# Kernel tuning notes

Measured on AMD Instinct MI355X. Metric: run time of the kernel, lower is better.

The kernel has to match this reference:

```python
import jax, jax.numpy as jnp
import numpy as np

STRIDE = 2
PADDING = (1, 1)
OUT_PADDING = (0, 0)


def conv_transpose2d(x, weight, bias, stride, padding, out_padding):
    # weight: (Cin, Cout, kh, kw) -- torch ConvTranspose2d layout.
    # The original code does: stride-insert zeros, zero-pad by (k-1), append
    # out_padding rows/cols, valid-conv with the spatially-flipped kernel,
    # then crop `padding` from each side. That is exactly a dilated conv:
    kh, kw = weight.shape[2], weight.shape[3]
    w = jnp.flip(weight, (2, 3)).transpose(1, 0, 2, 3)  # (Cout, Cin, kh, kw)
    pad = ((kh - 1 - padding[0], kh - 1 - padding[0] + out_padding[0]),
           (kw - 1 - padding[1], kw - 1 - padding[1] + out_padding[1]))
    out = jax.lax.conv_general_dilated(
        x, w,
        window_strides=(1, 1),
        padding=pad,
        lhs_dilation=(stride, stride),
        dimension_numbers=('NCHW', 'OIHW', 'NCHW'))
    return out + bias[None, :, None, None]


def setup_inputs() -> dict:
    key = jax.random.key(0)
    k1, k2, k3 = jax.random.split(key, 3)
    Cin, Cout, kh, kw = 256, 128, 4, 4
    bnd = (1.0 / (Cin * kh * kw)) ** 0.5  # matches uniform_(-k**0.5, k**0.5)
    x = jax.random.normal(k1, (16, Cin, 64, 64), dtype=jnp.float32)
    weight = jax.random.uniform(k2, (Cin, Cout, kh, kw), jnp.float32, -bnd, bnd)
    bias = jax.random.uniform(k3, (Cout,), jnp.float32, -bnd, bnd)
    return {"x": x, "weight": weight, "bias": bias}


def reference(x, weight, bias):
    # Output: (16, 128, 128, 128) = (H-1)*2 - 2*1 + 4
    return conv_transpose2d(x, weight, bias, STRIDE, PADDING, OUT_PADDING)
```

## Files before the change

### kernel.cpp

```cpp
#include <hip/hip_runtime.h>
#include <stdint.h>

typedef unsigned short u16;
typedef __bf16 bf16x8 __attribute__((ext_vector_type(8)));
typedef float f32x4 __attribute__((ext_vector_type(4)));
typedef float f32x2 __attribute__((ext_vector_type(2)));

static const size_t XT_BYTES = (size_t)16 * 66 * 66 * 256 * 2;
static const size_t WK_BYTES = (size_t)2 * 2 * 8 * 2 * 2 * 128 * 32 * 2;

__device__ __forceinline__ u16 f2bf(float f) {
  unsigned u = __float_as_uint(f);
  unsigned r = (u + 0x7fff + ((u >> 16) & 1)) >> 16;
  return (u16)r;
}

__device__ __forceinline__ void ld_g2l16(const u16* g, void* l) {
  __builtin_amdgcn_global_load_lds(
      (const __attribute__((address_space(1))) unsigned int*)(uintptr_t)g,
      (__attribute__((address_space(3))) unsigned int*)(unsigned int)(uintptr_t)l,
      16, 0, 0);
}

__device__ __forceinline__ int swz4(int row) { return (row ^ (row >> 2)) & 3; }

__global__ __launch_bounds__(256) void prep_all(const float* __restrict__ x,
                                                const float* __restrict__ w,
                                                u16* __restrict__ xt,
                                                u16* __restrict__ wk) {
  __shared__ __align__(16) u16 sh[64 * 264];
  const int t = threadIdx.x;
  const int bx = blockIdx.x;
  if (bx >= 1056) {
    int id = (bx - 1056) * 256 + t;
    int ci5 = id & 31;
    int co = (id >> 5) & 127;
    int q = (id >> 12) & 1;
    int dw = (id >> 13) & 1;
    int kc = (id >> 14) & 7;
    int dh = (id >> 17) & 1;
    int p = id >> 18;
    int ci = kc * 32 + ci5;
    int kh = 2 * dh + 1 - p;
    int kw = 2 * dw + 1 - q;
    wk[id] = f2bf(w[((ci * 128 + co) * 4 + kh) * 4 + kw]);
    return;
  }
  const int n = bx / 66;
  const int ihp = bx - n * 66;
  u16* xtn = xt + ((size_t)(n * 66 + ihp)) * 66 * 256;
  if (ihp == 0 || ihp == 65) {
    for (int j = 0; j < 9; ++j) {
      int idx = j * 256 + t;
      if (idx < 2112) ((uint4*)xtn)[idx] = make_uint4(0, 0, 0, 0);
    }
    return;
  }
  const int ih = ihp - 1;
  const int iw0 = (t & 15) * 4;
  const int cb = (t >> 4) * 4;
  const int swz = (t & 3) << 3;
  const float* xb = x + (size_t)n * 1048576 + (size_t)ih * 64 + iw0;
#pragma unroll
  for (int it = 0; it < 4; ++it) {
    int ci0 = it * 64 + cb;
    float4 v0 = *(const float4*)(xb + (size_t)(ci0 + 0) * 4096);
    float4 v1 = *(const float4*)(xb + (size_t)(ci0 + 1) * 4096);
    float4 v2 = *(const float4*)(xb + (size_t)(ci0 + 2) * 4096);
    float4 v3 = *(const float4*)(xb + (size_t)(ci0 + 3) * 4096);
    int col = ci0 ^ swz;
    ushort4 u;
    u.x = f2bf(v0.x); u.y = f2bf(v1.x); u.z = f2bf(v2.x); u.w = f2bf(v3.x);
    *(ushort4*)&sh[(iw0 + 0) * 264 + col] = u;
    u.x = f2bf(v0.y); u.y = f2bf(v1.y); u.z = f2bf(v2.y); u.w = f2bf(v3.y);
    *(ushort4*)&sh[(iw0 + 1) * 264 + col] = u;
    u.x = f2bf(v0.z); u.y = f2bf(v1.z); u.z = f2bf(v2.z); u.w = f2bf(v3.z);
    *(ushort4*)&sh[(iw0 + 2) * 264 + col] = u;
    u.x = f2bf(v0.w); u.y = f2bf(v1.w); u.z = f2bf(v2.w); u.w = f2bf(v3.w);
    *(ushort4*)&sh[(iw0 + 3) * 264 + col] = u;
  }
  __syncthreads();
#pragma unroll
  for (int j = 0; j < 8; ++j) {
    int idx = j * 256 + t;
    int iw = idx >> 5;
    int chunk = idx & 31;
    uint4 v = *(const uint4*)&sh[iw * 264 + ((chunk ^ ((iw >> 2) & 3)) << 3)];
    *(uint4*)&xtn[(size_t)(iw + 1) * 256 + chunk * 8] = v;
  }
  if (t < 64) {
    int iwp = (t >> 5) * 65;
    int chunk = t & 31;
    *(uint4*)&xtn[(size_t)iwp * 256 + chunk * 8] = make_uint4(0, 0, 0, 0);
  }
}

__global__ __launch_bounds__(512, 2) void gemm_ct(const u16* __restrict__ xt,
                                                  const u16* __restrict__ wk,
                                                  const float* __restrict__ bias,
                                                  float* __restrict__ out) {
  __shared__ __align__(16) u16 As[2][16384];
  __shared__ __align__(16) u16 Bs[2][8448];
  const int t = threadIdx.x;
  const int lane = t & 63;
  const int wv = t >> 6;
  const int wm = wv >> 2, wr = wv & 3;
  const int quad = lane >> 4, l15 = lane & 15;

  const int id = blockIdx.x;
  const int sid = (id & 7) * 64 + (id >> 3);
  const int mt = sid & 15;
  const int n = (sid >> 4) & 15;
  const int p = sid >> 8;
  const int m0 = mt * 4;

  const u16* wkp = wk + (size_t)p * 262144;
  const u16* xtn = xt + (size_t)n * (66 * 66 * 256);

  int aoffs[4];
#pragma unroll
  for (int it = 0; it < 4; ++it) {
    int c = it * 512 + t;
    int rr = c >> 2;
    aoffs[it] = rr * 32 + ((c & 3) ^ swz4(rr & 127)) * 8;
  }
  int bsrc[3];
#pragma unroll
  for (int it = 0; it < 3; ++it) {
    int c = it * 512 + t;
    int rr = c / 264;
    int rem = c - 264 * rr;
    int iwp = rem >> 2;
    bsrc[it] = rr * 16896 + iwp * 256 + ((rem & 3) ^ swz4(iwp)) * 8;
  }

  int aoff[4];
#pragma unroll
  for (int i = 0; i < 4; ++i) {
    int co = wm * 64 + i * 16 + l15;
    aoff[i] = co * 32 + (quad ^ swz4(co)) * 8;
  }
  int bro[3][4];
#pragma unroll
  for (int k = 0; k < 3; ++k)
#pragma unroll
    for (int j = 0; j < 4; ++j) {
      int b0 = j * 16 + l15 + k;
      bro[k][j] = wr * 2112 + b0 * 32 + (quad ^ swz4(b0)) * 8;
    }

  f32x4 acc[2][4][4];
#pragma unroll
  for (int q = 0; q < 2; ++q)
#pragma unroll
    for (int i = 0; i < 4; ++i)
#pragma unroll
      for (int j = 0; j < 4; ++j) acc[q][i][j] = (f32x4){0.f, 0.f, 0.f, 0.f};

  auto stage = [&](int buf, int pr) {
    const int kc = pr & 7, dh = pr >> 3;
    const u16* asrc = wkp + (size_t)(dh * 8 + kc) * 16384;
    u16* Ad = &As[buf][0];
#pragma unroll
    for (int it = 0; it < 4; ++it)
      ld_g2l16(asrc + aoffs[it], Ad + (it * 512 + t) * 8);
    const u16* bbase = xtn + (size_t)(m0 + p - dh + 1) * 16896 + kc * 32;
    u16* Bd = &Bs[buf][0];
    ld_g2l16(bbase + bsrc[0], Bd + t * 8);
    ld_g2l16(bbase + bsrc[1], Bd + (512 + t) * 8);
    if (t < 32) ld_g2l16(bbase + bsrc[2], Bd + (1024 + t) * 8);
  };

#define MFMA16(ACC, AF, BF)                                              \
  do {                                                                   \
    _Pragma("unroll") for (int i = 0; i < 4; ++i)                        \
        _Pragma("unroll") for (int j = 0; j < 4; ++j)                    \
        ACC[i][j] = __builtin_amdgcn_mfma_f32_16x16x32_bf16(             \
            AF[i], BF[j], ACC[i][j], 0, 0, 0);                           \
  } while (0)

  stage(0, 0);
  asm volatile("s_waitcnt vmcnt(0)" ::: "memory");
  __builtin_amdgcn_s_barrier();
  asm volatile("" ::: "memory");

#pragma unroll 2
  for (int pr = 0; pr < 16; ++pr) {
    const u16* Ac = &As[pr & 1][0];
    const u16* Bc = &Bs[pr & 1][0];
    if (pr < 15) stage((pr + 1) & 1, pr + 1);
    __builtin_amdgcn_sched_barrier(0);
    bf16x8 keep[4], bx[4], af[4];
#pragma unroll
    for (int j = 0; j < 4; ++j) keep[j] = *(const bf16x8*)(Bc + bro[1][j]);
#pragma unroll
    for (int i = 0; i < 4; ++i) af[i] = *(const bf16x8*)(Ac + aoff[i]);
    __builtin_amdgcn_s_setprio(1);
    MFMA16(acc[0], af, keep);
    __builtin_amdgcn_s_setprio(0);
    __builtin_amdgcn_sched_barrier(0);
#pragma unroll
    for (int j = 0; j < 4; ++j) bx[j] = *(const bf16x8*)(Bc + bro[2][j]);
#pragma unroll
    for (int i = 0; i < 4; ++i) af[i] = *(const bf16x8*)(Ac + 4096 + aoff[i]);
    __builtin_amdgcn_s_setprio(1);
    MFMA16(acc[1], af, bx);
    __builtin_amdgcn_s_setprio(0);
    __builtin_amdgcn_sched_barrier(0);
#pragma unroll
    for (int j = 0; j < 4; ++j) bx[j] = *(const bf16x8*)(Bc + bro[0][j]);
#pragma unroll
    for (int i = 0; i < 4; ++i) af[i] = *(const bf16x8*)(Ac + 8192 + aoff[i]);
    __builtin_amdgcn_s_setprio(1);
    MFMA16(acc[0], af, bx);
    __builtin_amdgcn_s_setprio(0);
    __builtin_amdgcn_sched_barrier(0);
#pragma unroll
    for (int i = 0; i < 4; ++i) af[i] = *(const bf16x8*)(Ac + 12288 + aoff[i]);
    __builtin_amdgcn_s_setprio(1);
    MFMA16(acc[1], af, keep);
    __builtin_amdgcn_s_setprio(0);
    asm volatile("s_waitcnt lgkmcnt(0) vmcnt(0)" ::: "memory");
    __builtin_amdgcn_s_barrier();
    asm volatile("" ::: "memory");
  }
#undef MFMA16

  const int oh = 2 * (m0 + wr) + p;
#pragma unroll
  for (int i = 0; i < 4; ++i) {
#pragma unroll
    for (int j = 0; j < 4; ++j) {
      int l = j * 16 + l15;
#pragma unroll
      for (int r = 0; r < 4; ++r) {
        int co = wm * 64 + i * 16 + quad * 4 + r;
        float bv = bias[co];
        f32x2 v;
        v.x = acc[0][i][j][r] + bv;
        v.y = acc[1][i][j][r] + bv;
        __builtin_nontemporal_store(
            v, (f32x2*)&out[(((size_t)n * 128 + co) * 128 + oh) * 128 + 2 * l]);
      }
    }
  }
}

__global__ __launch_bounds__(256) void ct_fallback(const float* __restrict__ x,
                                                   const float* __restrict__ w,
                                                   const float* __restrict__ bias,
                                                   float* __restrict__ out) {
  size_t id = (size_t)blockIdx.x * 256 + threadIdx.x;
  if (id >= (size_t)16 * 128 * 128 * 128) return;
  int ow = (int)(id & 127), oh = (int)(id >> 7) & 127;
  int co = (int)(id >> 14) & 127, n = (int)(id >> 21);
  int pp = oh & 1, m = oh >> 1, qq = ow & 1, l = ow >> 1;
  float s = bias[co];
  for (int ci = 0; ci < 256; ++ci) {
    for (int dh = 0; dh < 2; ++dh) {
      int ih = m + pp - dh;
      if (ih < 0 || ih > 63) continue;
      int kh = 2 * dh + 1 - pp;
      for (int dw = 0; dw < 2; ++dw) {
        int iw = l + qq - dw;
        if (iw < 0 || iw > 63) continue;
        int kw = 2 * dw + 1 - qq;
        s += x[(((size_t)n * 256 + ci) * 64 + ih) * 64 + iw] *
             w[((ci * 128 + co) * 4 + kh) * 4 + kw];
      }
    }
  }
  out[id] = s;
}

extern "C" void kernel_launch(void* const* d_in, const int* in_sizes, int n_in,
                              void* d_out, int out_size, void* d_ws, size_t ws_size,
                              hipStream_t stream) {
  const float* x = (const float*)d_in[0];
  const float* w = (const float*)d_in[1];
  const float* bias = (const float*)d_in[2];
  float* out = (float*)d_out;
  if (ws_size >= XT_BYTES + WK_BYTES) {
    u16* xt = (u16*)d_ws;
    u16* wkb = (u16*)((char*)d_ws + XT_BYTES);
    hipLaunchKernelGGL(prep_all, dim3(3104), dim3(256), 0, stream, x, w, xt, wkb);
    hipLaunchKernelGGL(gemm_ct, dim3(512), dim3(512), 0, stream, xt, wkb, bias, out);
  } else {
    hipLaunchKernelGGL(ct_fallback, dim3(131072), dim3(256), 0, stream, x, w, bias, out);
  }
}
```

Measured before the change: 241.6 us.

## Triple-buffer B tile, prefetch two stages ahead, reorder block-to-tile mapping

Splits the staging of weights (A) and input (B) so that B is triple-buffered and prefetched two iterations ahead while A stays double-buffered. The barrier moves to the top of the loop with partial vmcnt waits, so the next loads can overlap the current MFMA work instead of draining everything each iteration. It also remaps block ids so that the parity index p varies fastest, which changes L2 locality for the input and weight tiles. The extra B buffer raises LDS use and may cut occupancy, and unroll drops to 1. The per-wave vmcnt counts are fragile.

```diff
diff --git a/kernel.cpp b/kernel.cpp
--- a/kernel.cpp
+++ b/kernel.cpp
@@ -100,7 +100,7 @@
                                                   const float* __restrict__ bias,
                                                   float* __restrict__ out) {
   __shared__ __align__(16) u16 As[2][16384];
-  __shared__ __align__(16) u16 Bs[2][8448];
+  __shared__ __align__(16) u16 Bs[3][8448];
   const int t = threadIdx.x;
   const int lane = t & 63;
   const int wv = t >> 6;
@@ -109,9 +109,9 @@
 
   const int id = blockIdx.x;
   const int sid = (id & 7) * 64 + (id >> 3);
-  const int mt = sid & 15;
-  const int n = (sid >> 4) & 15;
-  const int p = sid >> 8;
+  const int p = sid & 1;
+  const int mt = (sid >> 1) & 15;
+  const int n = (sid >> 5) & 15;
   const int m0 = mt * 4;
 
   const u16* wkp = wk + (size_t)p * 262144;
@@ -157,13 +157,15 @@
 #pragma unroll
       for (int j = 0; j < 4; ++j) acc[q][i][j] = (f32x4){0.f, 0.f, 0.f, 0.f};
 
-  auto stage = [&](int buf, int pr) {
-    const int kc = pr & 7, dh = pr >> 3;
-    const u16* asrc = wkp + (size_t)(dh * 8 + kc) * 16384;
+  auto stageA = [&](int buf, int pr) {
+    const u16* asrc = wkp + (size_t)pr * 16384;
     u16* Ad = &As[buf][0];
 #pragma unroll
     for (int it = 0; it < 4; ++it)
       ld_g2l16(asrc + aoffs[it], Ad + (it * 512 + t) * 8);
+  };
+  auto stageB = [&](int buf, int pr) {
+    const int kc = pr & 7, dh = pr >> 3;
     const u16* bbase = xtn + (size_t)(m0 + p - dh + 1) * 16896 + kc * 32;
     u16* Bd = &Bs[buf][0];
     ld_g2l16(bbase + bsrc[0], Bd + t * 8);
@@ -179,50 +181,55 @@
             AF[i], BF[j], ACC[i][j], 0, 0, 0);                           \
   } while (0)
 
-  stage(0, 0);
-  asm volatile("s_waitcnt vmcnt(0)" ::: "memory");
-  __builtin_amdgcn_s_barrier();
-  asm volatile("" ::: "memory");
-
-#pragma unroll 2
+  stageA(0, 0);
+  stageB(0, 0);
+  stageB(1, 1);
+
+#pragma unroll 1
   for (int pr = 0; pr < 16; ++pr) {
-    const u16* Ac = &As[pr & 1][0];
-    const u16* Bc = &Bs[pr & 1][0];
-    if (pr < 15) stage((pr + 1) & 1, pr + 1);
-    __builtin_amdgcn_sched_barrier(0);
-    bf16x8 keep[4], bx[4], af[4];
-#pragma unroll
-    for (int j = 0; j < 4; ++j) keep[j] = *(const bf16x8*)(Bc + bro[1][j]);
-#pragma unroll
-    for (int i = 0; i < 4; ++i) af[i] = *(const bf16x8*)(Ac + aoff[i]);
-    __builtin_amdgcn_s_setprio(1);
-    MFMA16(acc[0], af, keep);
-    __builtin_amdgcn_s_setprio(0);
-    __builtin_amdgcn_sched_barrier(0);
-#pragma unroll
-    for (int j = 0; j < 4; ++j) bx[j] = *(const bf16x8*)(Bc + bro[2][j]);
-#pragma unroll
-    for (int i = 0; i < 4; ++i) af[i] = *(const bf16x8*)(Ac + 4096 + aoff[i]);
-    __builtin_amdgcn_s_setprio(1);
-    MFMA16(acc[1], af, bx);
-    __builtin_amdgcn_s_setprio(0);
-    __builtin_amdgcn_sched_barrier(0);
-#pragma unroll
-    for (int j = 0; j < 4; ++j) bx[j] = *(const bf16x8*)(Bc + bro[0][j]);
-#pragma unroll
-    for (int i = 0; i < 4; ++i) af[i] = *(const bf16x8*)(Ac + 8192 + aoff[i]);
-    __builtin_amdgcn_s_setprio(1);
-    MFMA16(acc[0], af, bx);
-    __builtin_amdgcn_s_setprio(0);
-    __builtin_amdgcn_sched_barrier(0);
-#pragma unroll
-    for (int i = 0; i < 4; ++i) af[i] = *(const bf16x8*)(Ac + 12288 + aoff[i]);
-    __builtin_amdgcn_s_setprio(1);
-    MFMA16(acc[1], af, keep);
-    __builtin_amdgcn_s_setprio(0);
-    asm volatile("s_waitcnt lgkmcnt(0) vmcnt(0)" ::: "memory");
+    if (pr < 15) {
+      if (wv == 0)
+        asm volatile("s_waitcnt lgkmcnt(0) vmcnt(3)" ::: "memory");
+      else
+        asm volatile("s_waitcnt lgkmcnt(0) vmcnt(2)" ::: "memory");
+    } else {
+      asm volatile("s_waitcnt lgkmcnt(0) vmcnt(0)" ::: "memory");
+    }
     __builtin_amdgcn_s_barrier();
     asm volatile("" ::: "memory");
+    if (pr < 15) stageA((pr + 1) & 1, pr + 1);
+    if (pr < 14) stageB((pr + 2) % 3, pr + 2);
+    __builtin_amdgcn_sched_barrier(0);
+
+    const u16* Ac = &As[pr & 1][0];
+    const u16* Bc = &Bs[pr % 3][0];
+    bf16x8 keep[4], bx[4], af[4];
+#pragma unroll
+    for (int j = 0; j < 4; ++j) keep[j] = *(const bf16x8*)(Bc + bro[1][j]);
+#pragma unroll
+    for (int i = 0; i < 4; ++i) af[i] = *(const bf16x8*)(Ac + aoff[i]);
+    __builtin_amdgcn_s_setprio(1);
+    MFMA16(acc[0], af, keep);
+    __builtin_amdgcn_s_setprio(0);
+#pragma unroll
+    for (int j = 0; j < 4; ++j) bx[j] = *(const bf16x8*)(Bc + bro[2][j]);
+#pragma unroll
+    for (int i = 0; i < 4; ++i) af[i] = *(const bf16x8*)(Ac + 4096 + aoff[i]);
+    __builtin_amdgcn_s_setprio(1);
+    MFMA16(acc[1], af, bx);
+    __builtin_amdgcn_s_setprio(0);
+#pragma unroll
+    for (int j = 0; j < 4; ++j) bx[j] = *(const bf16x8*)(Bc + bro[0][j]);
+#pragma unroll
+    for (int i = 0; i < 4; ++i) af[i] = *(const bf16x8*)(Ac + 8192 + aoff[i]);
+    __builtin_amdgcn_s_setprio(1);
+    MFMA16(acc[0], af, bx);
+    __builtin_amdgcn_s_setprio(0);
+#pragma unroll
+    for (int i = 0; i < 4; ++i) af[i] = *(const bf16x8*)(Ac + 12288 + aoff[i]);
+    __builtin_amdgcn_s_setprio(1);
+    MFMA16(acc[1], af, keep);
+    __builtin_amdgcn_s_setprio(0);
   }
 #undef MFMA16
 
```

Result: no change. 242.7 us (+0.5%).
